# Kernel tuning notes

Hardware: AMD Instinct MI355X
Metric: run time of the kernel (lower is better)

## Reference

```python
import jax, jax.numpy as jnp
import numpy as np

B, T, H, I, O = 64, 1024, 512, 64, 8
NOISE_STD = 0.05
ALPHA = 0.2


def setup_inputs() -> dict:
    key = jax.random.key(0)
    ks = jax.random.split(key, 5)
    return {
        "input": jax.random.normal(ks[0], (B, T, I), dtype=jnp.float32),
        "noise": jax.random.normal(ks[1], (B, T, H), dtype=jnp.float32),
        "wi": jax.random.normal(ks[2], (I, H), dtype=jnp.float32) / np.float32(np.sqrt(H)),
        "si": jnp.ones((I,), jnp.float32),
        # scale so the all-positive effective recurrence |wrec| stays stable over T steps
        "wrec": jax.random.normal(ks[3], (H, H), dtype=jnp.float32) * np.float32(0.5 / H),
        "b": jnp.zeros((H,), jnp.float32),
        "wo": jax.random.normal(ks[4], (H, O), dtype=jnp.float32) / np.float32(H),
        "so": jnp.ones((O,), jnp.float32),
        "wi_mask": jnp.ones((I, H), jnp.float32),
        "wrec_mask": jnp.ones((H, H), jnp.float32),
        "wo_mask": jnp.ones((H, O), jnp.float32),
        "h0": jnp.zeros((H,), jnp.float32),
    }


def reference(input, noise, wi, si, wrec, b, wo, so, wi_mask, wrec_mask, wo_mask, h0):
    batch = input.shape[0]
    # effective weights (constant across timesteps; torch recomputes identical values each step)
    wrec_eff = jnp.abs(wrec) * wrec_mask            # [H, H]
    wi_eff = (wi * si[:, None]) * wi_mask           # [I, H]
    wo_eff = (wo * so[None, :]) * wo_mask           # [H, O]

    h_init = jnp.broadcast_to(h0, (batch, h0.shape[0]))  # [B, H]

    def step(h, xs):
        x_t, n_t = xs                                # [B, I], [B, H]
        r = jax.nn.relu(h)                           # rate from previous state
        h_new = h + NOISE_STD * n_t + ALPHA * (-h + r @ wrec_eff + b + x_t @ wi_eff)
        out_t = jax.nn.relu(h_new) @ wo_eff          # [B, O]
        return h_new, (out_t, h_new)

    xs = (jnp.swapaxes(input, 0, 1), jnp.swapaxes(noise, 0, 1))  # time-major
    _, (outs, hs) = jax.lax.scan(step, h_init, xs)
    output = jnp.swapaxes(outs, 0, 1)                            # [B, T, O]
    trajectories = jnp.concatenate(
        [h_init[:, None, :], jnp.swapaxes(hs, 0, 1)], axis=1     # [B, T+1, H]
    )
    return output, trajectories
```

## Files before the change

### kernel.cpp

```cpp
#include <hip/hip_runtime.h>
#include <hip/hip_bf16.h>
#include <cstddef>
#include <cstdint>

#define BB 64
#define TT 1024
#define HH 512
#define II 64
#define OO 8
#define NOISE_STD 0.05f
#define ALPHA 0.2f

#define G_SLICES 16
#define BT 4
#define NC (BB/BT)
#define K4EXT 160
#define R2STRIDE 328

typedef _Float16 half2_t __attribute__((ext_vector_type(2)));
typedef unsigned int uint32;
typedef uint32 uint4_t __attribute__((ext_vector_type(4)));

#if __has_builtin(__builtin_amdgcn_fdot2)
__device__ __forceinline__ float fdot2f(half2_t a, half2_t b, float c) {
    return __builtin_amdgcn_fdot2(a, b, c, false);
}
#else
__device__ __forceinline__ float fdot2f(half2_t a, half2_t b, float c) {
    return c + (float)a[0] * (float)b[0] + (float)a[1] * (float)b[1];
}
#endif

__device__ __forceinline__ half2_t pkrtz(float a, float b) {
    return __builtin_bit_cast(half2_t, __builtin_amdgcn_cvt_pkrtz(a, b));
}

__device__ __forceinline__ uint4_t load4_sc1(const uint32* p) {
    uint4_t v;
    asm volatile("global_load_dwordx4 %0, %1, off sc1\n\t"
                 "s_waitcnt vmcnt(0)"
                 : "=v"(v) : "v"(p) : "memory");
    return v;
}

__global__ __launch_bounds__(512, 2)
void rnn_clique(const float* __restrict__ input, const float* __restrict__ noise,
                const float* __restrict__ wi, const float* __restrict__ si,
                const float* __restrict__ wrec, const float* __restrict__ bvec,
                const float* __restrict__ wo, const float* __restrict__ so,
                const float* __restrict__ wi_mask, const float* __restrict__ wrec_mask,
                const float* __restrict__ wo_mask, const float* __restrict__ h0,
                uint32* __restrict__ ex, float* __restrict__ out,
                float* __restrict__ traj)
{
    const int tid  = threadIdx.x;
    const int cq   = blockIdx.x >> 4;
    const int sl   = blockIdx.x & 15;
    const int wv   = tid >> 6;
    const int lane = tid & 63;

    __shared__ half2_t w2[K4EXT * 64];
    __shared__ half2_t r2[BT][R2STRIDE];
    __shared__ float   part[BT][8][32];
    __shared__ half2_t wo2[256];

    {
        const int c = tid & 31, kg = tid >> 5;
        const int gc = sl * 32 + c;
        for (int m = 0; m < 10; ++m) {
            int k4 = m * 16 + kg;
            float v[4];
            #pragma unroll
            for (int q = 0; q < 4; ++q) {
                int kap = k4 * 4 + q;
                float x;
                if (kap < HH) {
                    x = fabsf(wrec[(size_t)kap * HH + gc]) * wrec_mask[(size_t)kap * HH + gc];
                } else if (kap < HH + II) {
                    int i = kap - HH;
                    x = wi[(size_t)i * HH + gc] * si[i] * wi_mask[(size_t)i * HH + gc];
                } else if (kap == HH + II) {
                    x = bvec[gc];
                } else {
                    x = 0.f;
                }
                v[q] = x;
            }
            w2[k4 * 64 + c * 2]     = pkrtz(v[0], v[1]);
            w2[k4 * 64 + c * 2 + 1] = pkrtz(v[2], v[3]);
        }
    }
    if (sl < OO && tid < 256) {
        int k2 = tid, o = sl;
        float v0 = wo[(size_t)(2 * k2) * OO + o] * so[o] * wo_mask[(size_t)(2 * k2) * OO + o];
        float v1 = wo[(size_t)(2 * k2 + 1) * OO + o] * so[o] * wo_mask[(size_t)(2 * k2 + 1) * OO + o];
        wo2[k2] = pkrtz(v0, v1);
    }
    if (tid < 128) {
        int k4 = tid;
        float v0 = fmaxf(h0[4 * k4 + 0], 0.f), v1 = fmaxf(h0[4 * k4 + 1], 0.f);
        float v2 = fmaxf(h0[4 * k4 + 2], 0.f), v3 = fmaxf(h0[4 * k4 + 3], 0.f);
        half2_t p0 = pkrtz(v0, v1), p1 = pkrtz(v2, v3);
        for (int b = 0; b < BT; ++b) { r2[b][2 * k4] = p0; r2[b][2 * k4 + 1] = p1; }
    }
    if (tid < BT) {
        r2[tid][288] = half2_t{(_Float16)1.f, (_Float16)0.f};
        for (int s = 289; s < R2STRIDE; ++s) r2[tid][s] = half2_t{(_Float16)0.f, (_Float16)0.f};
    }
    if (wv >= 4 && lane < 32) {
        int b = wv - 4, i2 = lane;
        const float* xp = input + ((size_t)(cq * BT + b) * TT + 0) * II + 2 * i2;
        r2[b][256 + i2] = pkrtz(xp[0], xp[1]);
    }

    float h_st = 0.f, n_reg = 0.f;
    float* trajp = nullptr;
    const float* noisep = nullptr;
    uint32* exw = nullptr;
    if (wv < BT && lane < 32) {
        int b = wv, c = lane, gc = sl * 32 + c, bg = cq * BT + b;
        h_st   = h0[gc];
        noisep = noise + (size_t)bg * TT * HH;
        trajp  = traj + (size_t)bg * (TT + 1) * HH;
        n_reg  = noisep[gc];
        trajp[gc] = h_st;
        exw = ex + (size_t)((cq * 2 + 0) * BT + b) * HH + gc;
    }
    __syncthreads();

    const int c_    = lane & 31;
    const int shalf = lane >> 5;
    const int seg   = wv * 2 + shalf;

    const int gb  = tid >> 7;
    const int k4g = tid & 127;
    uint32* exg0 = ex + (size_t)((cq * 2 + 0) * BT + gb) * HH + (size_t)(4 * k4g);
    const size_t expar = (size_t)BT * HH;

    for (int t = 0; t < TT; ++t) {
        float acc0 = 0.f, acc1 = 0.f, acc2 = 0.f, acc3 = 0.f;
        #pragma unroll
        for (int ch = 0; ch < 5; ++ch) {
            int k2b = seg * 20 + ch * 4;
            int k4b = seg * 10 + ch * 2;
            half2_t w00 = w2[k4b * 64 + c_ * 2];
            half2_t w01 = w2[k4b * 64 + c_ * 2 + 1];
            half2_t w10 = w2[(k4b + 1) * 64 + c_ * 2];
            half2_t w11 = w2[(k4b + 1) * 64 + c_ * 2 + 1];
            {
                half2_t ra = r2[0][k2b], rb = r2[0][k2b + 1], rc = r2[0][k2b + 2], rd = r2[0][k2b + 3];
                acc0 = fdot2f(ra, w00, acc0); acc0 = fdot2f(rb, w01, acc0);
                acc0 = fdot2f(rc, w10, acc0); acc0 = fdot2f(rd, w11, acc0);
            }
            {
                half2_t ra = r2[1][k2b], rb = r2[1][k2b + 1], rc = r2[1][k2b + 2], rd = r2[1][k2b + 3];
                acc1 = fdot2f(ra, w00, acc1); acc1 = fdot2f(rb, w01, acc1);
                acc1 = fdot2f(rc, w10, acc1); acc1 = fdot2f(rd, w11, acc1);
            }
            {
                half2_t ra = r2[2][k2b], rb = r2[2][k2b + 1], rc = r2[2][k2b + 2], rd = r2[2][k2b + 3];
                acc2 = fdot2f(ra, w00, acc2); acc2 = fdot2f(rb, w01, acc2);
                acc2 = fdot2f(rc, w10, acc2); acc2 = fdot2f(rd, w11, acc2);
            }
            {
                half2_t ra = r2[3][k2b], rb = r2[3][k2b + 1], rc = r2[3][k2b + 2], rd = r2[3][k2b + 3];
                acc3 = fdot2f(ra, w00, acc3); acc3 = fdot2f(rb, w01, acc3);
                acc3 = fdot2f(rc, w10, acc3); acc3 = fdot2f(rd, w11, acc3);
            }
        }
        acc0 += __shfl_xor(acc0, 32);
        acc1 += __shfl_xor(acc1, 32);
        acc2 += __shfl_xor(acc2, 32);
        acc3 += __shfl_xor(acc3, 32);
        if (shalf == 0) {
            part[0][wv][c_] = acc0;
            part[1][wv][c_] = acc1;
            part[2][wv][c_] = acc2;
            part[3][wv][c_] = acc3;
        }
        __syncthreads();

        const uint32 tag = (uint32)(t + 1);
        const size_t poff = (size_t)((t + 1) & 1) * expar;

        if (wv < BT && lane < 32) {
            int b = wv, c = lane, gc = sl * 32 + c;
            float mv = 0.f;
            #pragma unroll
            for (int m = 0; m < 8; ++m) mv += part[b][m][c];
            float hn = (1.f - ALPHA) * h_st + ALPHA * mv + NOISE_STD * n_reg;
            h_st = hn;
            uint32 r16 = __builtin_bit_cast(uint32,
                           __builtin_amdgcn_cvt_pkrtz(fmaxf(hn, 0.f), 0.f)) & 0xFFFFu;
            uint32 word = (tag << 16) | r16;
            __hip_atomic_store(exw + poff, word,
                               __ATOMIC_RELAXED, __HIP_MEMORY_SCOPE_AGENT);
            trajp[(size_t)(t + 1) * HH + gc] = hn;
            int tn = (t + 1 < TT) ? (t + 1) : (TT - 1);
            n_reg = noisep[(size_t)tn * HH + gc];
        } else if (wv >= 4) {
            if (sl < OO && t > 0) {
                int b = wv - 4;
                int k2 = lane * 4;
                float p = 0.f;
                p = fdot2f(r2[b][k2],     wo2[k2],     p);
                p = fdot2f(r2[b][k2 + 1], wo2[k2 + 1], p);
                p = fdot2f(r2[b][k2 + 2], wo2[k2 + 2], p);
                p = fdot2f(r2[b][k2 + 3], wo2[k2 + 3], p);
                #pragma unroll
                for (int d = 32; d >= 1; d >>= 1) p += __shfl_xor(p, d);
                if (lane == 0) out[((size_t)(cq * BT + b) * TT + (t - 1)) * OO + sl] = p;
            }
            if (lane < 32) {
                int b = wv - 4, i2 = lane;
                int tn = (t + 1 < TT) ? (t + 1) : (TT - 1);
                const float* xp = input + ((size_t)(cq * BT + b) * TT + tn) * II + 2 * i2;
                r2[b][256 + i2] = pkrtz(xp[0], xp[1]);
            }
        }
        __syncthreads();

        {
            const uint32* g0 = exg0 + poff;
            uint4_t w;
            for (;;) {
                w = load4_sc1(g0);
                if ((w[0] >> 16) == tag && (w[1] >> 16) == tag &&
                    (w[2] >> 16) == tag && (w[3] >> 16) == tag) break;
                __builtin_amdgcn_s_sleep(1);
            }
            uint32 p0 = (w[0] & 0xFFFFu) | (w[1] << 16);
            uint32 p1 = (w[2] & 0xFFFFu) | (w[3] << 16);
            r2[gb][2 * k4g]     = __builtin_bit_cast(half2_t, p0);
            r2[gb][2 * k4g + 1] = __builtin_bit_cast(half2_t, p1);
        }
        __syncthreads();
    }

    if (wv >= 4 && sl < OO) {
        int b = wv - 4;
        int k2 = lane * 4;
        float p = 0.f;
        p = fdot2f(r2[b][k2],     wo2[k2],     p);
        p = fdot2f(r2[b][k2 + 1], wo2[k2 + 1], p);
        p = fdot2f(r2[b][k2 + 2], wo2[k2 + 2], p);
        p = fdot2f(r2[b][k2 + 3], wo2[k2 + 3], p);
        #pragma unroll
        for (int d = 32; d >= 1; d >>= 1) p += __shfl_xor(p, d);
        if (lane == 0) out[((size_t)(cq * BT + b) * TT + (TT - 1)) * OO + sl] = p;
    }
}

extern "C" void kernel_launch(void* const* d_in, const int* in_sizes, int n_in,
                              void* d_out, int out_size, void* d_ws, size_t ws_size,
                              hipStream_t stream) {
    const float* input     = (const float*)d_in[0];
    const float* noise     = (const float*)d_in[1];
    const float* wi        = (const float*)d_in[2];
    const float* si        = (const float*)d_in[3];
    const float* wrec      = (const float*)d_in[4];
    const float* bvec      = (const float*)d_in[5];
    const float* wo        = (const float*)d_in[6];
    const float* so        = (const float*)d_in[7];
    const float* wi_mask   = (const float*)d_in[8];
    const float* wrec_mask = (const float*)d_in[9];
    const float* wo_mask   = (const float*)d_in[10];
    const float* h0        = (const float*)d_in[11];

    float* out  = (float*)d_out;
    float* traj = out + (size_t)BB * TT * OO;
    uint32* ex  = (uint32*)d_ws;

    (void)hipMemsetAsync(d_ws, 0, (size_t)NC * 2 * BT * HH * 4, stream);

    rnn_clique<<<dim3(NC * G_SLICES), dim3(512), 0, stream>>>(
        input, noise, wi, si, wrec, bvec, wo, so,
        wi_mask, wrec_mask, wo_mask, h0, ex, out, traj);
}
```

Before: 1.802 ms.

## Map each clique onto one XCD and use L2-local exchange when co-resident

Changes the block-to-(clique, slice) mapping so the 16 slices of one clique get round-robin-adjacent block ids and are likely placed on the same XCD. Each block records its XCC id, and the clique checks whether all members share one. If they do, the per-step exchange uses plain stores and sc0 loads that stay in the local L2 instead of going through device-coherent paths. This aims to cut inter-block synchronization latency per timestep, at the cost of a startup handshake and dependence on hardware block placement.

```diff
diff --git a/kernel.cpp b/kernel.cpp
--- a/kernel.cpp
+++ b/kernel.cpp
@@ -41,6 +41,16 @@
                  "s_waitcnt vmcnt(0)"
                  : "=v"(v) : "v"(p) : "memory");
     return v;
+}
+__device__ __forceinline__ uint4_t load4_sc0(const uint32* p) {
+    uint4_t v;
+    asm volatile("global_load_dwordx4 %0, %1, off sc0\n\t"
+                 "s_waitcnt vmcnt(0)"
+                 : "=v"(v) : "v"(p) : "memory");
+    return v;
+}
+__device__ __forceinline__ void store1_plain(uint32* p, uint32 v) {
+    asm volatile("global_store_dword %0, %1, off" :: "v"(p), "v"(v) : "memory");
 }
 
 __global__ __launch_bounds__(512, 2)
@@ -54,8 +64,8 @@
                 float* __restrict__ traj)
 {
     const int tid  = threadIdx.x;
-    const int cq   = blockIdx.x >> 4;
-    const int sl   = blockIdx.x & 15;
+    const int cq   = blockIdx.x & 15;
+    const int sl   = blockIdx.x >> 4;
     const int wv   = tid >> 6;
     const int lane = tid & 63;
 
@@ -63,6 +73,17 @@
     __shared__ half2_t r2[BT][R2STRIDE];
     __shared__ float   part[BT][8][32];
     __shared__ half2_t wo2[256];
+    __shared__ int     mode_sh;
+
+    uint32* aux = ex + (size_t)NC * 2 * BT * HH;
+
+    if (tid == 0) {
+        uint32 xcc;
+        asm volatile("s_getreg_b32 %0, hwreg(HW_REG_XCC_ID)" : "=s"(xcc));
+        xcc &= 0xFFu;
+        __hip_atomic_store(aux + cq * 16 + sl, (1u << 16) | xcc,
+                           __ATOMIC_RELAXED, __HIP_MEMORY_SCOPE_AGENT);
+    }
 
     {
         const int c = tid & 31, kg = tid >> 5;
@@ -126,7 +147,23 @@
         trajp[gc] = h_st;
         exw = ex + (size_t)((cq * 2 + 0) * BT + b) * HH + gc;
     }
+
+    if (wv == 0) {
+        uint32 v = (1u << 16);
+        for (;;) {
+            if (lane < 16)
+                v = __hip_atomic_load(aux + cq * 16 + lane,
+                                      __ATOMIC_RELAXED, __HIP_MEMORY_SCOPE_AGENT);
+            if (__ballot((v >> 16) == 1u) == ~0ull) break;
+            __builtin_amdgcn_s_sleep(1);
+        }
+        uint32 myx = v & 0xFFFFu;
+        uint32 x0  = __shfl(myx, 0);
+        bool eq = (lane < 16) ? (myx == x0) : true;
+        if (lane == 0) mode_sh = (__ballot(eq) == ~0ull) ? 1 : 0;
+    }
     __syncthreads();
+    const bool local_mode = (mode_sh != 0);
 
     const int c_    = lane & 31;
     const int shalf = lane >> 5;
@@ -193,8 +230,12 @@
             uint32 r16 = __builtin_bit_cast(uint32,
                            __builtin_amdgcn_cvt_pkrtz(fmaxf(hn, 0.f), 0.f)) & 0xFFFFu;
             uint32 word = (tag << 16) | r16;
-            __hip_atomic_store(exw + poff, word,
-                               __ATOMIC_RELAXED, __HIP_MEMORY_SCOPE_AGENT);
+            if (local_mode) {
+                store1_plain(exw + poff, word);
+            } else {
+                __hip_atomic_store(exw + poff, word,
+                                   __ATOMIC_RELAXED, __HIP_MEMORY_SCOPE_AGENT);
+            }
             trajp[(size_t)(t + 1) * HH + gc] = hn;
             int tn = (t + 1 < TT) ? (t + 1) : (TT - 1);
             n_reg = noisep[(size_t)tn * HH + gc];
@@ -223,11 +264,20 @@
         {
             const uint32* g0 = exg0 + poff;
             uint4_t w;
-            for (;;) {
-                w = load4_sc1(g0);
-                if ((w[0] >> 16) == tag && (w[1] >> 16) == tag &&
-                    (w[2] >> 16) == tag && (w[3] >> 16) == tag) break;
-                __builtin_amdgcn_s_sleep(1);
+            if (local_mode) {
+                for (;;) {
+                    w = load4_sc0(g0);
+                    if ((w[0] >> 16) == tag && (w[1] >> 16) == tag &&
+                        (w[2] >> 16) == tag && (w[3] >> 16) == tag) break;
+                    __builtin_amdgcn_s_sleep(1);
+                }
+            } else {
+                for (;;) {
+                    w = load4_sc1(g0);
+                    if ((w[0] >> 16) == tag && (w[1] >> 16) == tag &&
+                        (w[2] >> 16) == tag && (w[3] >> 16) == tag) break;
+                    __builtin_amdgcn_s_sleep(1);
+                }
             }
             uint32 p0 = (w[0] & 0xFFFFu) | (w[1] << 16);
             uint32 p1 = (w[2] & 0xFFFFu) | (w[3] << 16);
@@ -271,7 +321,8 @@
     float* traj = out + (size_t)BB * TT * OO;
     uint32* ex  = (uint32*)d_ws;
 
-    (void)hipMemsetAsync(d_ws, 0, (size_t)NC * 2 * BT * HH * 4, stream);
+    (void)hipMemsetAsync(d_ws, 0,
+        (size_t)(NC * 2 * BT * HH + NC * G_SLICES) * sizeof(uint32), stream);
 
     rnn_clique<<<dim3(NC * G_SLICES), dim3(512), 0, stream>>>(
         input, noise, wi, si, wrec, bvec, wo, so,
```

After: 1.689 ms. 1.07x faster.
